# Kernel optimization log

Hardware: AMD Instinct MI355X
Metric: run time of the kernel (lower is better)

## Reference

```python
import jax, jax.numpy as jnp
import numpy as np

B, L, E, H, K = 256, 500, 300, 10, 5  # batch, doc_len, word_embedding, h1, num_aspects


def setup_inputs() -> dict:
    key = jax.random.key(0)
    k1, k2, k3 = jax.random.split(key, 3)
    review = jax.random.normal(k1, (B, L, E), dtype=jnp.float32)
    # params initialized uniform(-0.01, 0.01) as in the torch module
    aspProj = jax.random.uniform(k2, (K, E, H), dtype=jnp.float32, minval=-0.01, maxval=0.01)
    aspEmbed = jax.random.uniform(k3, (K, 3 * H), dtype=jnp.float32, minval=-0.01, maxval=0.01)
    return {"review": review, "aspProj": aspProj, "aspEmbed": aspEmbed}


def reference(review, aspProj, aspEmbed):
    # project review into each aspect subspace: (K, B, L, H)
    proj = jnp.einsum('ble,keh->kblh', review, aspProj)
    # pad seq dim by 1 on each side, build window-3 unfold.
    # torch unfold(1,3,1) yields (B, L, H, 3) then reshape to (B, L, 3*H),
    # i.e. feature layout is (h_index, window_offset) -- match by stacking
    # window offsets on the LAST axis before the reshape.
    padded = jnp.pad(proj, ((0, 0), (0, 0), (1, 1), (0, 0)))
    windows = jnp.stack([padded[:, :, i:i + L, :] for i in range(3)], axis=-1)  # (K,B,L,H,3)
    windows = windows.reshape(K, windows.shape[1], L, 3 * H)  # (K,B,L,3H)
    # attention logits per position, softmax over the WHOLE sequence dim
    scores = jnp.einsum('kblf,kf->kbl', windows, aspEmbed)
    attn = jax.nn.softmax(scores, axis=-1)  # (K,B,L)
    # attention-weighted sum over sequence -> aspect representation
    rep = jnp.einsum('kblh,kbl->kbh', proj, attn)  # (K,B,H)
    batch_aspAttn = jnp.transpose(attn, (1, 0, 2))  # (B,K,L)
    batch_aspRep = jnp.transpose(rep, (1, 0, 2))    # (B,K,H)
    return (batch_aspAttn, batch_aspRep)
```

## Files before the change

### kernel.cpp

```cpp
#include <hip/hip_runtime.h>

#define BB 256
#define LL 500
#define EE 300
#define HH 10
#define KK 5
#define NF 50
#define NT 512
#define NWAVE 8

#define MP 512
#define CK 64
#define NCH 5
#define AP 72
#define BP 328
#define PP 53

#define A_BYTES   (MP * AP * 2)
#define B_OFF     A_BYTES
#define SD_OFF    (MP * PP * 4)
#define RED_OFF   (SD_OFF + 3 * KK * MP * 4)
#define REP_OFF   (RED_OFF + KK * NWAVE * 4)
#define EMB_OFF   (REP_OFF + NWAVE * NF * 4)
#define SMEM_BYTES (EMB_OFF + KK * 3 * HH * 4)

typedef __attribute__((ext_vector_type(8))) short short8;
typedef __attribute__((ext_vector_type(4))) float f32x4;

__device__ __forceinline__ unsigned short f2bf(float x) {
    unsigned int u = __float_as_uint(x);
    return (unsigned short)((u + 0x7FFFu + ((u >> 16) & 1u)) >> 16);
}

__global__ __launch_bounds__(NT, 2) void anr_mfma(
    const float* __restrict__ review,
    const float* __restrict__ aspProj,
    const float* __restrict__ aspEmbed,
    float* __restrict__ out)
{
    __shared__ __align__(16) char smem[SMEM_BYTES];
    short* A16   = (short*)smem;
    short* B16   = (short*)(smem + B_OFF);
    float* proj  = (float*)smem;
    float* s_d   = (float*)(smem + SD_OFF);
    float* s_red = (float*)(smem + RED_OFF);
    float* s_rep = (float*)(smem + REP_OFF);
    float* s_emb = (float*)(smem + EMB_OFF);

    const int tid  = threadIdx.x;
    const int b    = blockIdx.x;
    const int lane = tid & 63;
    const int w    = tid >> 6;
    const int quad = lane >> 4;
    const int m16  = lane & 15;

    for (int j = tid; j < (64 * BP * 2) / 4; j += NT)
        ((int*)(smem + B_OFF))[j] = 0;
    if (tid < KK * 3 * HH) s_emb[tid] = aspEmbed[tid];
    __syncthreads();

    const float4* rev4 = (const float4*)review + (size_t)b * LL * (EE / 4);
    const int q  = tid & 15;
    const int r0 = tid >> 4;
    float4 pre[16];
#pragma unroll
    for (int i = 0; i < 16; ++i) {
        int r = 32 * i + r0;
        float4 z = {0.f, 0.f, 0.f, 0.f};
        pre[i] = (r < LL && q < EE / 4) ? rev4[(size_t)r * (EE / 4) + q] : z;
    }
    for (int j = tid; j < KK * EE * HH; j += NT) {
        int kasp = j / (EE * HH);
        int rr   = j - kasp * (EE * HH);
        int e    = rr / HH;
        int h    = rr - e * HH;
        B16[(kasp * HH + h) * BP + e] = (short)f2bf(aspProj[j]);
    }

    f32x4 acc[4][4];
#pragma unroll
    for (int mi = 0; mi < 4; ++mi)
#pragma unroll
        for (int ni = 0; ni < 4; ++ni)
            acc[mi][ni] = (f32x4){0.f, 0.f, 0.f, 0.f};

    for (int c = 0; c < NCH; ++c) {
        __syncthreads();
#pragma unroll
        for (int i = 0; i < 16; ++i) {
            int r = 32 * i + r0;
            float4 v = pre[i];
            uint2 pk;
            pk.x = (unsigned)f2bf(v.x) | ((unsigned)f2bf(v.y) << 16);
            pk.y = (unsigned)f2bf(v.z) | ((unsigned)f2bf(v.w) << 16);
            *(uint2*)&A16[r * AP + q * 4] = pk;
        }
        __syncthreads();
        if (c + 1 < NCH) {
#pragma unroll
            for (int i = 0; i < 16; ++i) {
                int r  = 32 * i + r0;
                int fq = (c + 1) * 16 + q;
                float4 z = {0.f, 0.f, 0.f, 0.f};
                pre[i] = (r < LL && fq < EE / 4) ? rev4[(size_t)r * (EE / 4) + fq] : z;
            }
        }
#pragma unroll
        for (int s = 0; s < 2; ++s) {
            short8 af[4], bf[4];
#pragma unroll
            for (int mi = 0; mi < 4; ++mi)
                af[mi] = *(const short8*)&A16[(w * 64 + mi * 16 + m16) * AP + s * 32 + quad * 8];
#pragma unroll
            for (int ni = 0; ni < 4; ++ni)
                bf[ni] = *(const short8*)&B16[(ni * 16 + m16) * BP + c * 64 + s * 32 + quad * 8];
#pragma unroll
            for (int mi = 0; mi < 4; ++mi)
#pragma unroll
                for (int ni = 0; ni < 4; ++ni)
                    acc[mi][ni] = __builtin_amdgcn_mfma_f32_16x16x32_bf16(
                        af[mi], bf[ni], acc[mi][ni], 0, 0, 0);
        }
    }

    __syncthreads();
#pragma unroll
    for (int mi = 0; mi < 4; ++mi) {
#pragma unroll
        for (int ni = 0; ni < 4; ++ni) {
            int col = ni * 16 + m16;
            if (col < NF) {
                int row = w * 64 + mi * 16 + quad * 4;
#pragma unroll
                for (int r = 0; r < 4; ++r)
                    proj[(row + r) * PP + col] = acc[mi][ni][r];
            }
        }
    }
    __syncthreads();

    const int l  = tid;
    const bool vl = (l < LL);

    float pr[NF];
#pragma unroll
    for (int f = 0; f < NF; ++f) pr[f] = proj[l * PP + f];

    float d0[KK], d1[KK], d2[KK];
#pragma unroll
    for (int k = 0; k < KK; ++k) {
        float a0 = 0.f, a1 = 0.f, a2 = 0.f;
#pragma unroll
        for (int h = 0; h < HH; ++h) {
            float x  = pr[k * HH + h];
            a0 = fmaf(x, s_emb[k * 3 * HH + 3 * h + 0], a0);
            a1 = fmaf(x, s_emb[k * 3 * HH + 3 * h + 1], a1);
            a2 = fmaf(x, s_emb[k * 3 * HH + 3 * h + 2], a2);
        }
        d0[k] = a0; d1[k] = a1; d2[k] = a2;
    }
#pragma unroll
    for (int k = 0; k < KK; ++k) {
        s_d[(0 * KK + k) * MP + l] = d0[k];
        s_d[(1 * KK + k) * MP + l] = d1[k];
        s_d[(2 * KK + k) * MP + l] = d2[k];
    }
    __syncthreads();

    const int lp1 = (l + 1 < MP) ? l + 1 : MP - 1;
    float sc[KK];
#pragma unroll
    for (int k = 0; k < KK; ++k) {
        float t0 = (l >= 1) ? s_d[(0 * KK + k) * MP + l - 1] : 0.f;
        float t1 = s_d[(1 * KK + k) * MP + l];
        float t2 = s_d[(2 * KK + k) * MP + lp1];
        sc[k] = vl ? (t0 + t1 + t2) : -1e30f;
    }

    float mx[KK];
#pragma unroll
    for (int k = 0; k < KK; ++k) {
        float m = sc[k];
        for (int s = 32; s > 0; s >>= 1) m = fmaxf(m, __shfl_xor(m, s, 64));
        if (lane == 0) s_red[k * NWAVE + w] = m;
    }
    __syncthreads();
#pragma unroll
    for (int k = 0; k < KK; ++k) {
        float m = s_red[k * NWAVE + 0];
#pragma unroll
        for (int ww = 1; ww < NWAVE; ++ww) m = fmaxf(m, s_red[k * NWAVE + ww]);
        mx[k] = m;
    }
    __syncthreads();
    float ex[KK], sm[KK];
#pragma unroll
    for (int k = 0; k < KK; ++k) {
        ex[k] = __expf(sc[k] - mx[k]);
        float s = ex[k];
        for (int sh = 32; sh > 0; sh >>= 1) s += __shfl_xor(s, sh, 64);
        if (lane == 0) s_red[k * NWAVE + w] = s;
    }
    __syncthreads();
#pragma unroll
    for (int k = 0; k < KK; ++k) {
        float s = 0.f;
#pragma unroll
        for (int ww = 0; ww < NWAVE; ++ww) s += s_red[k * NWAVE + ww];
        sm[k] = s;
    }

#pragma unroll
    for (int k = 0; k < KK; ++k) {
        float wk = ex[k] / sm[k];
        if (vl) out[((size_t)b * KK + k) * LL + l] = wk;
#pragma unroll
        for (int h = 0; h < HH; ++h) {
            float v = pr[k * HH + h] * wk;
            for (int sh = 32; sh > 0; sh >>= 1) v += __shfl_xor(v, sh, 64);
            if (lane == 0) s_rep[w * NF + k * HH + h] = v;
        }
    }
    __syncthreads();
    if (tid < NF) {
        float s = 0.f;
#pragma unroll
        for (int ww = 0; ww < NWAVE; ++ww) s += s_rep[ww * NF + tid];
        out[(size_t)BB * KK * LL + (size_t)b * NF + tid] = s;
    }
}

extern "C" void kernel_launch(void* const* d_in, const int* in_sizes, int n_in,
                              void* d_out, int out_size, void* d_ws, size_t ws_size,
                              hipStream_t stream) {
    const float* review   = (const float*)d_in[0];
    const float* aspProj  = (const float*)d_in[1];
    const float* aspEmbed = (const float*)d_in[2];
    float* out = (float*)d_out;

    anr_mfma<<<dim3(BB), dim3(NT), 0, stream>>>(review, aspProj, aspEmbed, out);
}
```

Before: 248.7 us.

## Double-buffer review tiles in LDS with smaller K-chunks and one barrier per chunk

The review staging moves from a single 64-wide LDS buffer to two 32-wide buffers. The next chunk is converted and stored while MFMAs run on the current one, so each chunk needs one barrier instead of two. The aspProj and aspEmbed loads are issued into registers up front so their global latency overlaps the first review loads. The trade-off is twice as many chunks, each with less MFMA work to hide load latency, plus more register pressure from the prefetched weights, which could reduce occupancy.

```diff
diff --git a/kernel.cpp b/kernel.cpp
--- a/kernel.cpp
+++ b/kernel.cpp
@@ -10,36 +10,36 @@
 #define NWAVE 8
 
 #define MP 512
-#define CK 64
-#define NCH 5
-#define AP 72
+#define CK 32
+#define NCH 10
+#define AP 40
 #define BP 328
 #define PP 53
 
-#define A_BYTES   (MP * AP * 2)
-#define B_OFF     A_BYTES
-#define SD_OFF    (MP * PP * 4)
-#define RED_OFF   (SD_OFF + 3 * KK * MP * 4)
-#define REP_OFF   (RED_OFF + KK * NWAVE * 4)
-#define EMB_OFF   (REP_OFF + NWAVE * NF * 4)
+#define A1_OFF   (MP * AP * 2)
+#define B_OFF    (2 * MP * AP * 2)
+#define B_BYTES  (64 * BP * 2)
+#define SD_OFF   (MP * PP * 4)
+#define RED_OFF  (SD_OFF + 3 * KK * MP * 4)
+#define REP_OFF  (RED_OFF + KK * NWAVE * 4)
+#define EMB_OFF  (REP_OFF + NWAVE * NF * 4)
 #define SMEM_BYTES (EMB_OFF + KK * 3 * HH * 4)
 
 typedef __attribute__((ext_vector_type(8))) short short8;
 typedef __attribute__((ext_vector_type(4))) float f32x4;
 
-__device__ __forceinline__ unsigned short f2bf(float x) {
+__device__ __forceinline__ unsigned int f2bf(float x) {
     unsigned int u = __float_as_uint(x);
-    return (unsigned short)((u + 0x7FFFu + ((u >> 16) & 1u)) >> 16);
+    return (u + 0x7FFFu + ((u >> 16) & 1u)) >> 16;
 }
 
-__global__ __launch_bounds__(NT, 2) void anr_mfma(
+__global__ __launch_bounds__(NT, 2) void anr_mfma2(
     const float* __restrict__ review,
     const float* __restrict__ aspProj,
     const float* __restrict__ aspEmbed,
     float* __restrict__ out)
 {
     __shared__ __align__(16) char smem[SMEM_BYTES];
-    short* A16   = (short*)smem;
     short* B16   = (short*)(smem + B_OFF);
     float* proj  = (float*)smem;
     float* s_d   = (float*)(smem + SD_OFF);
@@ -53,29 +53,55 @@
     const int w    = tid >> 6;
     const int quad = lane >> 4;
     const int m16  = lane & 15;
-
-    for (int j = tid; j < (64 * BP * 2) / 4; j += NT)
+    const int q    = tid & 7;
+    const int r0   = tid >> 3;
+
+    for (int j = tid; j < B_BYTES / 4; j += NT)
         ((int*)(smem + B_OFF))[j] = 0;
-    if (tid < KK * 3 * HH) s_emb[tid] = aspEmbed[tid];
-    __syncthreads();
+    __syncthreads();
+
+    float btv[30];
+#pragma unroll
+    for (int i = 0; i < 30; ++i) {
+        int j = tid + NT * i;
+        btv[i] = (j < KK * EE * HH) ? aspProj[j] : 0.f;
+    }
+    float embv = (tid < KK * 3 * HH) ? aspEmbed[tid] : 0.f;
 
     const float4* rev4 = (const float4*)review + (size_t)b * LL * (EE / 4);
-    const int q  = tid & 15;
-    const int r0 = tid >> 4;
-    float4 pre[16];
-#pragma unroll
-    for (int i = 0; i < 16; ++i) {
-        int r = 32 * i + r0;
+    float4 ld[8];
+#pragma unroll
+    for (int i = 0; i < 8; ++i) {
+        int r = r0 + 64 * i;
         float4 z = {0.f, 0.f, 0.f, 0.f};
-        pre[i] = (r < LL && q < EE / 4) ? rev4[(size_t)r * (EE / 4) + q] : z;
-    }
-    for (int j = tid; j < KK * EE * HH; j += NT) {
-        int kasp = j / (EE * HH);
-        int rr   = j - kasp * (EE * HH);
-        int e    = rr / HH;
-        int h    = rr - e * HH;
-        B16[(kasp * HH + h) * BP + e] = (short)f2bf(aspProj[j]);
-    }
+        ld[i] = (r < LL) ? rev4[(size_t)r * 75 + q] : z;
+    }
+
+#pragma unroll
+    for (int i = 0; i < 30; ++i) {
+        int j = tid + NT * i;
+        if (j < KK * EE * HH) {
+            int kasp = j / (EE * HH);
+            int rr   = j - kasp * (EE * HH);
+            int e    = rr / HH;
+            int h    = rr - e * HH;
+            B16[(kasp * HH + h) * BP + e] = (short)f2bf(btv[i]);
+        }
+    }
+    if (tid < KK * 3 * HH) s_emb[tid] = embv;
+
+    {
+        short* An = (short*)smem;
+#pragma unroll
+        for (int i = 0; i < 8; ++i) {
+            int r = r0 + 64 * i;
+            uint2 pk;
+            pk.x = f2bf(ld[i].x) | (f2bf(ld[i].y) << 16);
+            pk.y = f2bf(ld[i].z) | (f2bf(ld[i].w) << 16);
+            *(uint2*)&An[r * AP + q * 4] = pk;
+        }
+    }
+    __syncthreads();
 
     f32x4 acc[4][4];
 #pragma unroll
@@ -84,42 +110,43 @@
         for (int ni = 0; ni < 4; ++ni)
             acc[mi][ni] = (f32x4){0.f, 0.f, 0.f, 0.f};
 
+#pragma unroll
     for (int c = 0; c < NCH; ++c) {
-        __syncthreads();
-#pragma unroll
-        for (int i = 0; i < 16; ++i) {
-            int r = 32 * i + r0;
-            float4 v = pre[i];
-            uint2 pk;
-            pk.x = (unsigned)f2bf(v.x) | ((unsigned)f2bf(v.y) << 16);
-            pk.y = (unsigned)f2bf(v.z) | ((unsigned)f2bf(v.w) << 16);
-            *(uint2*)&A16[r * AP + q * 4] = pk;
-        }
-        __syncthreads();
         if (c + 1 < NCH) {
-#pragma unroll
-            for (int i = 0; i < 16; ++i) {
-                int r  = 32 * i + r0;
-                int fq = (c + 1) * 16 + q;
+            const int fqB = (c + 1) * 8;
+#pragma unroll
+            for (int i = 0; i < 8; ++i) {
+                int r = r0 + 64 * i;
                 float4 z = {0.f, 0.f, 0.f, 0.f};
-                pre[i] = (r < LL && fq < EE / 4) ? rev4[(size_t)r * (EE / 4) + fq] : z;
+                ld[i] = (r < LL && (fqB + q) < EE / 4)
+                            ? rev4[(size_t)r * 75 + fqB + q] : z;
             }
         }
-#pragma unroll
-        for (int s = 0; s < 2; ++s) {
-            short8 af[4], bf[4];
-#pragma unroll
-            for (int mi = 0; mi < 4; ++mi)
-                af[mi] = *(const short8*)&A16[(w * 64 + mi * 16 + m16) * AP + s * 32 + quad * 8];
+        const short* Ac = (const short*)smem + (c & 1) * (MP * AP);
+        short8 af[4], bf[4];
+#pragma unroll
+        for (int mi = 0; mi < 4; ++mi)
+            af[mi] = *(const short8*)&Ac[(w * 64 + mi * 16 + m16) * AP + quad * 8];
+#pragma unroll
+        for (int ni = 0; ni < 4; ++ni)
+            bf[ni] = *(const short8*)&B16[(ni * 16 + m16) * BP + c * CK + quad * 8];
+#pragma unroll
+        for (int mi = 0; mi < 4; ++mi)
 #pragma unroll
             for (int ni = 0; ni < 4; ++ni)
-                bf[ni] = *(const short8*)&B16[(ni * 16 + m16) * BP + c * 64 + s * 32 + quad * 8];
-#pragma unroll
-            for (int mi = 0; mi < 4; ++mi)
-#pragma unroll
-                for (int ni = 0; ni < 4; ++ni)
-                    acc[mi][ni] = __builtin_amdgcn_mfma_f32_16x16x32_bf16(
-                        af[mi], bf[ni], acc[mi][ni], 0, 0, 0);
+                acc[mi][ni] = __builtin_amdgcn_mfma_f32_16x16x32_bf16(
+                    af[mi], bf[ni], acc[mi][ni], 0, 0, 0);
+        if (c + 1 < NCH) {
+            short* An = (short*)smem + ((c + 1) & 1) * (MP * AP);
+#pragma unroll
+            for (int i = 0; i < 8; ++i) {
+                int r = r0 + 64 * i;
+                uint2 pk;
+                pk.x = f2bf(ld[i].x) | (f2bf(ld[i].y) << 16);
+                pk.y = f2bf(ld[i].z) | (f2bf(ld[i].w) << 16);
+                *(uint2*)&An[r * AP + q * 4] = pk;
+            }
+            __syncthreads();
         }
     }
 
@@ -152,7 +179,7 @@
         float a0 = 0.f, a1 = 0.f, a2 = 0.f;
 #pragma unroll
         for (int h = 0; h < HH; ++h) {
-            float x  = pr[k * HH + h];
+            float x = pr[k * HH + h];
             a0 = fmaf(x, s_emb[k * 3 * HH + 3 * h + 0], a0);
             a1 = fmaf(x, s_emb[k * 3 * HH + 3 * h + 1], a1);
             a2 = fmaf(x, s_emb[k * 3 * HH + 3 * h + 2], a2);
@@ -238,5 +265,5 @@
     const float* aspEmbed = (const float*)d_in[2];
     float* out = (float*)d_out;
 
-    anr_mfma<<<dim3(BB), dim3(NT), 0, stream>>>(review, aspProj, aspEmbed, out);
+    anr_mfma2<<<dim3(BB), dim3(NT), 0, stream>>>(review, aspProj, aspEmbed, out);
 }
```

After: 247.5 us. No clear change (-0.5%).
